# Performance work log

Measured on AMD Instinct MI355X. Metric: run time of the kernel, lower is better.

## Reference

```python
import jax, jax.numpy as jnp
import numpy as np
from jax import lax

B = 8192      # image batch
S = 32        # seq_length
I = 16        # ltc_input_size (sensory neurons)
U = 19        # ltc_hidden_size (units)
M = 2         # num_classes (motor neurons)
UNFOLDS = 6   # ncps LTCCell default ode_unfolds
EPS = 1e-8


def setup_inputs() -> dict:
    key = jax.random.key(0)
    ks = jax.random.split(key, 24)
    u = lambda k, sh, lo, hi: jax.random.uniform(k, sh, jnp.float32, lo, hi)
    x = jax.random.normal(ks[0], (B, 1, 28, 44), jnp.float32)
    conv1_w = jax.random.normal(ks[1], (6, 1, 5, 5), jnp.float32) * 0.2
    conv1_b = u(ks[2], (6,), -0.1, 0.1)
    conv2_w = jax.random.normal(ks[3], (16, 6, 5, 5), jnp.float32) * 0.08
    conv2_b = u(ks[4], (16,), -0.1, 0.1)
    # wiring adjacency (AutoNCP approximated by random sparse +/-1 polarity)
    sparsity_mask = (jax.random.uniform(ks[5], (U, U)) < 0.5).astype(jnp.float32)
    sensory_sparsity_mask = (jax.random.uniform(ks[6], (I, U)) < 0.5).astype(jnp.float32)
    erev = sparsity_mask * jnp.where(jax.random.uniform(ks[7], (U, U)) < 0.8, 1.0, -1.0)
    sensory_erev = sensory_sparsity_mask * jnp.where(jax.random.uniform(ks[8], (I, U)) < 0.8, 1.0, -1.0)
    # LTCCell parameter init ranges from ncps
    gleak = u(ks[9], (U,), 0.001, 1.0)
    vleak = u(ks[10], (U,), -0.2, 0.2)
    cm = u(ks[11], (U,), 0.4, 0.6)
    sigma = u(ks[12], (U, U), 3.0, 8.0)
    mu = u(ks[13], (U, U), 0.3, 0.8)
    w = u(ks[14], (U, U), 0.001, 1.0)
    sensory_sigma = u(ks[15], (I, U), 3.0, 8.0)
    sensory_mu = u(ks[16], (I, U), 0.3, 0.8)
    sensory_w = u(ks[17], (I, U), 0.001, 1.0)
    input_w = jnp.ones((I,), jnp.float32)
    input_b = jnp.zeros((I,), jnp.float32)
    output_w = jnp.ones((M,), jnp.float32)
    output_b = jnp.zeros((M,), jnp.float32)
    return dict(x=x, conv1_w=conv1_w, conv1_b=conv1_b, conv2_w=conv2_w, conv2_b=conv2_b,
                gleak=gleak, vleak=vleak, cm=cm, sigma=sigma, mu=mu, w=w, erev=erev,
                sensory_sigma=sensory_sigma, sensory_mu=sensory_mu, sensory_w=sensory_w,
                sensory_erev=sensory_erev, input_w=input_w, input_b=input_b,
                output_w=output_w, output_b=output_b,
                sparsity_mask=sparsity_mask, sensory_sparsity_mask=sensory_sparsity_mask)


def _maxpool2(h):
    return lax.reduce_window(h, -jnp.inf, lax.max, (1, 1, 2, 2), (1, 1, 2, 2), 'VALID')


def reference(x, conv1_w, conv1_b, conv2_w, conv2_b, gleak, vleak, cm, sigma, mu, w,
              erev, sensory_sigma, sensory_mu, sensory_w, sensory_erev, input_w, input_b,
              output_w, output_b, sparsity_mask, sensory_sparsity_mask):
    dn = ('NCHW', 'OIHW', 'NCHW')
    h = lax.conv_general_dilated(x, conv1_w, (1, 1), 'VALID', dimension_numbers=dn)
    h = _maxpool2(jax.nn.relu(h + conv1_b[None, :, None, None]))
    h = lax.conv_general_dilated(h, conv2_w, (1, 1), 'VALID', dimension_numbers=dn)
    h = _maxpool2(jax.nn.relu(h + conv2_b[None, :, None, None]))
    feat = h.reshape(h.shape[0], -1).reshape(-1, S, I)   # (B, 32, 16)
    seq = jnp.swapaxes(feat, 0, 1)                       # (S, B, I)
    cm_t = cm * UNFOLDS                                  # cm / (elapsed_time/unfolds), dt=1

    def step(v, inp):
        inp = inp * input_w + input_b                    # sensory affine mapping
        # sensory synapse activations (B, I, U), fixed over the ODE unfolds
        s_act = sensory_w * jax.nn.sigmoid(sensory_sigma * (inp[:, :, None] - sensory_mu))
        s_act = s_act * sensory_sparsity_mask
        w_num_s = jnp.sum(s_act * sensory_erev, axis=1)
        w_den_s = jnp.sum(s_act, axis=1)

        def unfold(vv, _):
            wa = w * jax.nn.sigmoid(sigma * (vv[:, :, None] - mu)) * sparsity_mask  # (B,U,U)
            num = cm_t * vv + gleak * vleak + jnp.sum(wa * erev, axis=1) + w_num_s
            den = cm_t + gleak + jnp.sum(wa, axis=1) + w_den_s
            return num / (den + EPS), None

        v, _ = lax.scan(unfold, v, None, length=UNFOLDS)
        return v, None

    v0 = jnp.zeros((feat.shape[0], U), x.dtype)
    vT, _ = lax.scan(step, v0, seq)
    # motor mapping: first M neurons, affine output map; equals out[:, -1, :]
    return vT[:, :M] * output_w + output_b
```

## Files before the change

### kernel.cpp

```cpp
#include <hip/hip_runtime.h>

#define BTOT 8192
#define SEQ 32
#define IPB 6
#define TPB 128
#define L2E 1.4426950408889634f
#define FSTRIDE 520
#define RSL 16


__global__ void prep_w2t(const float* __restrict__ w2, float* __restrict__ wt) {
    int idx = blockIdx.x * blockDim.x + threadIdx.x;
    if (idx < 2400) {
        int k = idx >> 4, c2 = idx & 15;
        wt[idx] = w2[c2 * 150 + k];
    }
}

__global__ void prep_params(
    const float* __restrict__ sigma, const float* __restrict__ mu,
    const float* __restrict__ ww, const float* __restrict__ erev,
    const float* __restrict__ ssigma, const float* __restrict__ smu,
    const float* __restrict__ sw, const float* __restrict__ serev,
    const float* __restrict__ inw, const float* __restrict__ inb,
    const float* __restrict__ mask, const float* __restrict__ smask,
    float* __restrict__ ws)
{
    __shared__ int mcol[19];
    float2* sAB = (float2*)(ws + 5632);
    float2* sZI = (float2*)(ws + 6240);
    int* cnt = (int*)(ws + 6848);
    float* Ap = ws + 7168;
    float* Bp = ws + 7680;
    float* Zp = ws + 8192;
    const int t = threadIdx.x;
    for (int idx = t; idx < 456; idx += 64) {
        int i = idx / 19, j = idx - (idx / 19) * 19;
        float a = 0.f, b = 0.f, z = 0.f;
        if (i < 19 && mask[i * 19 + j] != 0.f) {
            float s = sigma[i * 19 + j];
            a = -L2E * s;
            b = L2E * s * mu[i * 19 + j];
            z = ww[i * 19 + j] * erev[i * 19 + j];
        }
        Ap[idx] = a; Bp[idx] = b; Zp[idx] = z;
    }
    if (t < 19) {
        const int j = t;
        for (int c = 0; c < 16; ++c) {
            sAB[c * 19 + j] = make_float2(0.f, 0.f);
            sZI[c * 19 + j] = make_float2(0.f, __int_as_float(0));
        }
        int c = 0;
        for (int i = 0; i < 16; ++i) {
            int idx = i * 19 + j;
            if (smask[idx] != 0.f) {
                float s = ssigma[idx];
                sAB[c * 19 + j] = make_float2(-L2E * s * inw[i],
                                              -L2E * s * (inb[i] - smu[idx]));
                sZI[c * 19 + j] = make_float2(sw[idx] * serev[idx], __int_as_float(i));
                ++c;
            }
        }
        mcol[j] = c;
    }
    __syncthreads();
    if (t == 0) {
        int MS = 0;
        for (int k = 0; k < 19; ++k) MS = max(MS, mcol[k]);
        cnt[0] = 0;
        cnt[1] = MS;
    }
}

__global__ __launch_bounds__(128, 4) void conv_k(
    const float* __restrict__ xin,
    const float* __restrict__ w1, const float* __restrict__ b1,
    const float* __restrict__ b2, const float* __restrict__ wt,
    const float* __restrict__ sparam,
    const int* __restrict__ cnt,
    float2* __restrict__ wnwd)
{
    __shared__ __align__(16) float img[1232];
    __shared__ __align__(16) float c1p[1440];
    const int tid = threadIdx.x;
    const int bG = blockIdx.x;

    for (int idx = tid; idx < 1232; idx += 128) img[idx] = xin[bG * 1232 + idx];
    __syncthreads();
    for (int idx = tid; idx < 240; idx += 128) {
        int y = idx / 20, xx = idx - (idx / 20) * 20;
        const float* ib = img + (2 * y) * 44 + 2 * xx;
        float win[6][6];
        #pragma unroll
        for (int r = 0; r < 6; ++r) {
            float2 a = *(const float2*)(ib + r * 44);
            float2 b = *(const float2*)(ib + r * 44 + 2);
            float2 c = *(const float2*)(ib + r * 44 + 4);
            win[r][0] = a.x; win[r][1] = a.y; win[r][2] = b.x;
            win[r][3] = b.y; win[r][4] = c.x; win[r][5] = c.y;
        }
        for (int ch = 0; ch < 6; ++ch) {
            const float* wp = w1 + ch * 25;
            float a00 = 0.f, a01 = 0.f, a10 = 0.f, a11 = 0.f;
            #pragma unroll
            for (int ky = 0; ky < 5; ++ky)
                #pragma unroll
                for (int kx = 0; kx < 5; ++kx) {
                    float wv = wp[ky * 5 + kx];
                    a00 = fmaf(wv, win[ky][kx], a00);
                    a01 = fmaf(wv, win[ky][kx + 1], a01);
                    a10 = fmaf(wv, win[ky + 1][kx], a10);
                    a11 = fmaf(wv, win[ky + 1][kx + 1], a11);
                }
            float m = fmaxf(fmaxf(a00, a01), fmaxf(a10, a11)) + b1[ch];
            c1p[ch * 240 + idx] = fmaxf(m, 0.f);
        }
    }
    __syncthreads();
    {
        const int oy = tid >> 4, ox = tid & 15;
        float acc[16];
        #pragma unroll
        for (int c2 = 0; c2 < 16; ++c2) acc[c2] = 0.f;
        for (int ch = 0; ch < 6; ++ch) {
            const float* rowb = c1p + ch * 240 + oy * 20 + ox;
            const float* wch = wt + (ch * 25 << 4);
            #pragma unroll
            for (int ky = 0; ky < 5; ++ky) {
                #pragma unroll
                for (int kx = 0; kx < 5; ++kx) {
                    float xv = rowb[ky * 20 + kx];
                    const float4* wk = (const float4*)(wch + ((ky * 5 + kx) << 4));
                    float4 wa = wk[0], wb = wk[1], wc = wk[2], wd = wk[3];
                    acc[0]  = fmaf(wa.x, xv, acc[0]);  acc[1]  = fmaf(wa.y, xv, acc[1]);
                    acc[2]  = fmaf(wa.z, xv, acc[2]);  acc[3]  = fmaf(wa.w, xv, acc[3]);
                    acc[4]  = fmaf(wb.x, xv, acc[4]);  acc[5]  = fmaf(wb.y, xv, acc[5]);
                    acc[6]  = fmaf(wb.z, xv, acc[6]);  acc[7]  = fmaf(wb.w, xv, acc[7]);
                    acc[8]  = fmaf(wc.x, xv, acc[8]);  acc[9]  = fmaf(wc.y, xv, acc[9]);
                    acc[10] = fmaf(wc.z, xv, acc[10]); acc[11] = fmaf(wc.w, xv, acc[11]);
                    acc[12] = fmaf(wd.x, xv, acc[12]); acc[13] = fmaf(wd.y, xv, acc[13]);
                    acc[14] = fmaf(wd.z, xv, acc[14]); acc[15] = fmaf(wd.w, xv, acc[15]);
                }
            }
        }
        const bool wl = ((tid & 1) == 0) && ((tid & 16) == 0);
        const int obase = (oy >> 1) * 8 + (ox >> 1);
        #pragma unroll
        for (int c2 = 0; c2 < 16; ++c2) {
            float a = acc[c2];
            a = fmaxf(a, __shfl_xor(a, 1));
            a = fmaxf(a, __shfl_xor(a, 16));
            if (wl) img[obase + c2 * 32] = fmaxf(a + b2[c2], 0.f);
        }
    }
    __syncthreads();
    for (int idx = tid; idx < 1216; idx += 128) c1p[idx] = sparam[idx];
    __syncthreads();
    {
        const float2* sAB2 = (const float2*)c1p;
        const float2* sZI2 = (const float2*)(c1p + 608);
        const float* featI = img;
        const int MS = cnt[1];
        for (int p = tid; p < 608; p += 128) {
            int st = p / 19, j = p - (p / 19) * 19;
            float wn = 0.f, wd = 0.f;
            for (int c = 0; c < MS; ++c) {
                float2 ab = sAB2[c * 19 + j];
                float2 zi = sZI2[c * 19 + j];
                float f = featI[st * 16 + __float_as_int(zi.y)];
                float t = fmaf(ab.x, f, ab.y);
                float r = __builtin_amdgcn_rcpf(1.f + __builtin_amdgcn_exp2f(t));
                wn = fmaf(zi.x, r, wn);
                wd = fmaf(fabsf(zi.x), r, wd);
            }
            wnwd[(bG * SEQ + st) * 19 + j] = make_float2(wn, wd);
        }
    }
}

__global__ __launch_bounds__(128, 6) void ltc_k2(
    const float2* __restrict__ wnwd,
    const float* __restrict__ Ap, const float* __restrict__ Bp,
    const float* __restrict__ Zp,
    const float* __restrict__ gleak, const float* __restrict__ vleak,
    const float* __restrict__ cm,
    const float* __restrict__ outw, const float* __restrict__ outb,
    float* __restrict__ dout)
{
    __shared__ __align__(16) float vbuf[2][24];
    const int tid = threadIdx.x;
    const int wv = tid >> 6, l = tid & 63;
    const int s3 = l / 19;
    const int s = (s3 < 2) ? s3 : 2;
    const int j = l - s3 * 19;
    const int base = s * 8;
    const int img = blockIdx.x * 2 + wv;

    float A[8], Bb[8], Z[8];
    #pragma unroll
    for (int c = 0; c < 8; ++c) {
        A[c]  = Ap[(base + c) * 19 + j];
        Bb[c] = Bp[(base + c) * 19 + j];
        Z[c]  = Zp[(base + c) * 19 + j];
    }
    #pragma unroll
    for (int c = 0; c < 8; ++c)
        asm volatile("" : "+v"(A[c]), "+v"(Bb[c]), "+v"(Z[c]));

    const float gl = gleak[j];
    const float gv = gl * vleak[j];
    const float cmt = cm[j] * 6.f;

    float v = 0.f;
    float* vrow = &vbuf[wv][0];
    if (l < 24) vrow[l] = 0.f;
    __builtin_amdgcn_wave_barrier();
    __asm__ volatile("" ::: "memory");

    const float2* wrow = wnwd + img * SEQ * 19 + j;
    float2 wcur = wrow[0];

    #pragma unroll 1
    for (int st = 0; st < SEQ; ++st) {
        float2 wnext = (st < SEQ - 1) ? wrow[(st + 1) * 19] : wcur;
        const float nb = gv + wcur.x;
        const float db = cmt + gl + wcur.y;
        #pragma unroll 1
        for (int u = 0; u < 6; ++u) {
            float4 va = *(const float4*)(vrow + base);
            float4 vbq = *(const float4*)(vrow + base + 4);
            float vv[8] = {va.x, va.y, va.z, va.w, vbq.x, vbq.y, vbq.z, vbq.w};
            float pn0 = 0.f, pd0 = 0.f, pn1 = 0.f, pd1 = 0.f;
            #pragma unroll
            for (int p = 0; p < 4; ++p) {
                int c = p * 2;
                float t0 = fmaf(A[c], vv[c], Bb[c]);
                float t1 = fmaf(A[c + 1], vv[c + 1], Bb[c + 1]);
                float q0 = 1.f + __builtin_amdgcn_exp2f(t0);
                float q1 = 1.f + __builtin_amdgcn_exp2f(t1);
                float rr = __builtin_amdgcn_rcpf(q0 * q1);
                float cn = fmaf(Z[c], q1, Z[c + 1] * q0);
                float cd = fmaf(fabsf(Z[c]), q1, fabsf(Z[c + 1]) * q0);
                if (p & 1) { pn1 = fmaf(cn, rr, pn1); pd1 = fmaf(cd, rr, pd1); }
                else       { pn0 = fmaf(cn, rr, pn0); pd0 = fmaf(cd, rr, pd0); }
            }
            float pn = pn0 + pn1, pd = pd0 + pd1;
            float pnA = __shfl(pn, l + 19), pnB = __shfl(pn, l + 38);
            float pdA = __shfl(pd, l + 19), pdB = __shfl(pd, l + 38);
            float num = fmaf(cmt, v, nb) + (pn + pnA + pnB);
            float den = db + (pd + pdA + pdB);
            v = num * __builtin_amdgcn_rcpf(den + 1e-8f);
            __builtin_amdgcn_wave_barrier();
            __asm__ volatile("" ::: "memory");
            if (l < 19) vrow[l] = v;
            __builtin_amdgcn_wave_barrier();
            __asm__ volatile("" ::: "memory");
        }
        wcur = wnext;
    }
    if (l < 2) dout[img * 2 + l] = fmaf(v, outw[l], outb[l]);
}

__global__ __launch_bounds__(TPB, 3) void ltc_fused(
    const float* __restrict__ xin,
    const float* __restrict__ w1, const float* __restrict__ b1,
    const float* __restrict__ b2,
    const float* __restrict__ gleak, const float* __restrict__ vleak, const float* __restrict__ cm,
    const float* __restrict__ sigma, const float* __restrict__ mu, const float* __restrict__ ww,
    const float* __restrict__ erev,
    const float* __restrict__ ssigma, const float* __restrict__ smu, const float* __restrict__ sw,
    const float* __restrict__ serev,
    const float* __restrict__ inw, const float* __restrict__ inb,
    const float* __restrict__ outw, const float* __restrict__ outb,
    const float* __restrict__ mask, const float* __restrict__ smask,
    const float* __restrict__ wt,
    float* __restrict__ dout)
{
    __shared__ __align__(16) float uni[2736];
    __shared__ __align__(16) float featL[IPB * FSTRIDE];
    __shared__ int ncol[19], mcol[19], cnts[2];

    float* img = uni;
    float* c1p = uni + 1232;
    float2* rAB = (float2*)uni;
    float2* rZI = (float2*)(uni + 760);
    float2* sAB = (float2*)(uni + 1520);
    float2* sZI = (float2*)(uni + 2128);

    const int tid = threadIdx.x;
    const int b0 = blockIdx.x * IPB;

    for (int k = 0; k < IPB; ++k) {
        const int bG = b0 + k;
        const bool valid = bG < BTOT;
        if (valid) {
            for (int idx = tid; idx < 1232; idx += TPB) img[idx] = xin[bG * 1232 + idx];
        }
        __syncthreads();
        if (valid) {
            for (int idx = tid; idx < 240; idx += TPB) {
                int y = idx / 20, xx = idx - (idx / 20) * 20;
                const float* ib = img + (2 * y) * 44 + 2 * xx;
                float win[6][6];
                #pragma unroll
                for (int r = 0; r < 6; ++r) {
                    float2 a = *(const float2*)(ib + r * 44);
                    float2 b = *(const float2*)(ib + r * 44 + 2);
                    float2 c = *(const float2*)(ib + r * 44 + 4);
                    win[r][0] = a.x; win[r][1] = a.y; win[r][2] = b.x;
                    win[r][3] = b.y; win[r][4] = c.x; win[r][5] = c.y;
                }
                for (int ch = 0; ch < 6; ++ch) {
                    const float* wp = w1 + ch * 25;
                    float a00 = 0.f, a01 = 0.f, a10 = 0.f, a11 = 0.f;
                    #pragma unroll
                    for (int ky = 0; ky < 5; ++ky)
                        #pragma unroll
                        for (int kx = 0; kx < 5; ++kx) {
                            float wv = wp[ky * 5 + kx];
                            a00 = fmaf(wv, win[ky][kx], a00);
                            a01 = fmaf(wv, win[ky][kx + 1], a01);
                            a10 = fmaf(wv, win[ky + 1][kx], a10);
                            a11 = fmaf(wv, win[ky + 1][kx + 1], a11);
                        }
                    float m = fmaxf(fmaxf(a00, a01), fmaxf(a10, a11)) + b1[ch];
                    c1p[ch * 240 + idx] = fmaxf(m, 0.f);
                }
            }
        }
        __syncthreads();
        if (valid) {
            const int oy = tid >> 4, ox = tid & 15;
            float acc[16];
            #pragma unroll
            for (int c2 = 0; c2 < 16; ++c2) acc[c2] = 0.f;
            for (int ch = 0; ch < 6; ++ch) {
                const float* rowb = c1p + ch * 240 + oy * 20 + ox;
                const float* wch = wt + (ch * 25 << 4);
                #pragma unroll
                for (int ky = 0; ky < 5; ++ky) {
                    #pragma unroll
                    for (int kx = 0; kx < 5; ++kx) {
                        float xv = rowb[ky * 20 + kx];
                        const float4* wk = (const float4*)(wch + ((ky * 5 + kx) << 4));
                        float4 wa = wk[0], wb = wk[1], wc = wk[2], wd = wk[3];
                        acc[0]  = fmaf(wa.x, xv, acc[0]);  acc[1]  = fmaf(wa.y, xv, acc[1]);
                        acc[2]  = fmaf(wa.z, xv, acc[2]);  acc[3]  = fmaf(wa.w, xv, acc[3]);
                        acc[4]  = fmaf(wb.x, xv, acc[4]);  acc[5]  = fmaf(wb.y, xv, acc[5]);
                        acc[6]  = fmaf(wb.z, xv, acc[6]);  acc[7]  = fmaf(wb.w, xv, acc[7]);
                        acc[8]  = fmaf(wc.x, xv, acc[8]);  acc[9]  = fmaf(wc.y, xv, acc[9]);
                        acc[10] = fmaf(wc.z, xv, acc[10]); acc[11] = fmaf(wc.w, xv, acc[11]);
                        acc[12] = fmaf(wd.x, xv, acc[12]); acc[13] = fmaf(wd.y, xv, acc[13]);
                        acc[14] = fmaf(wd.z, xv, acc[14]); acc[15] = fmaf(wd.w, xv, acc[15]);
                    }
                }
            }
            const bool wl = ((tid & 1) == 0) && ((tid & 16) == 0);
            const int obase = k * FSTRIDE + (oy >> 1) * 8 + (ox >> 1);
            #pragma unroll
            for (int c2 = 0; c2 < 16; ++c2) {
                float a = acc[c2];
                a = fmaxf(a, __shfl_xor(a, 1));
                a = fmaxf(a, __shfl_xor(a, 16));
                if (wl) featL[obase + c2 * 32] = fmaxf(a + b2[c2], 0.f);
            }
        }
        __syncthreads();
    }

    for (int idx = tid; idx < 2736; idx += TPB) uni[idx] = 0.f;
    __syncthreads();
    if (tid < 19) {
        const int jj = tid;
        int c = 0;
        for (int i = 0; i < 19; ++i) {
            int idx = i * 19 + jj;
            if (mask[idx] != 0.f) {
                float s = sigma[idx];
                rAB[c * 19 + jj] = make_float2(-L2E * s, L2E * s * mu[idx]);
                rZI[c * 19 + jj] = make_float2(ww[idx] * erev[idx], __int_as_float(i));
                ++c;
            }
        }
        ncol[jj] = c;
        c = 0;
        for (int i = 0; i < 16; ++i) {
            int idx = i * 19 + jj;
            if (smask[idx] != 0.f) {
                float s = ssigma[idx];
                sAB[c * 19 + jj] = make_float2(-L2E * s * inw[i],
                                               -L2E * s * (inb[i] - smu[idx]));
                sZI[c * 19 + jj] = make_float2(sw[idx] * serev[idx], __int_as_float(i));
                ++c;
            }
        }
        mcol[jj] = c;
    }
    __syncthreads();
    if (tid == 0) {
        int MRv = 0, MSv = 0;
        for (int j2 = 0; j2 < 19; ++j2) {
            MRv = max(MRv, ncol[j2]);
            MSv = max(MSv, mcol[j2]);
        }
        cnts[0] = MRv;
        cnts[1] = MSv;
    }
    __syncthreads();
    const int MR = __builtin_amdgcn_readfirstlane(cnts[0]);
    const int MS = __builtin_amdgcn_readfirstlane(cnts[1]);

    const int wv_ = tid >> 6, l = tid & 63;
    const int g = l / 19;
    const int j = l - g * 19;
    const int gbase = g * 19;
    const int kimg = wv_ * 3 + g;
    const bool act = (g < 3) && (b0 + kimg < BTOT);
    const int kc = (kimg < IPB) ? kimg : (IPB - 1);

    float UA[RSL], UB[RSL], UZ[RSL];
    int LI[RSL];
    #pragma unroll
    for (int c = 0; c < RSL; ++c) {
        float2 ab = rAB[c * 19 + j];
        float2 zi = rZI[c * 19 + j];
        UA[c] = ab.x; UB[c] = ab.y; UZ[c] = zi.x;
        LI[c] = gbase + __float_as_int(zi.y);
    }
    #pragma unroll
    for (int c = 0; c < RSL; ++c)
        asm volatile("" : "+v"(UA[c]), "+v"(UB[c]), "+v"(UZ[c]), "+v"(LI[c]));

    const float gl = gleak[j];
    const float gv = gl * vleak[j];
    const float cmt = cm[j] * 6.f;

    float v = 0.f;
    const float* frow = featL + kc * FSTRIDE;

    #pragma unroll 1
    for (int st = 0; st < SEQ; ++st) {
        const float* fb = frow + st * 16;
        float wns = 0.f, wds = 0.f;
        #pragma unroll 1
        for (int c = 0; c < MS; ++c) {
            float2 ab = sAB[c * 19 + j];
            float2 zi = sZI[c * 19 + j];
            float f = fb[__float_as_int(zi.y)];
            float t = fmaf(ab.x, f, ab.y);
            float r = __builtin_amdgcn_rcpf(1.f + __builtin_amdgcn_exp2f(t));
            wns = fmaf(zi.x, r, wns);
            wds = fmaf(fabsf(zi.x), r, wds);
        }
        const float nb = gv + wns;
        const float db = cmt + gl + wds;
        #pragma unroll 1
        for (int u = 0; u < 6; ++u) {
            float num = fmaf(cmt, v, nb);
            float den = db;
            #pragma unroll
            for (int c = 0; c < RSL; ++c) {
                float vv = __shfl(v, LI[c]);
                float t = fmaf(UA[c], vv, UB[c]);
                float r = __builtin_amdgcn_rcpf(1.f + __builtin_amdgcn_exp2f(t));
                num = fmaf(UZ[c], r, num);
                den = fmaf(fabsf(UZ[c]), r, den);
            }
            #pragma unroll 1
            for (int c = RSL; c < MR; ++c) {
                float2 ab = rAB[c * 19 + j];
                float2 zi = rZI[c * 19 + j];
                float vv = __shfl(v, gbase + __float_as_int(zi.y));
                float t = fmaf(ab.x, vv, ab.y);
                float r = __builtin_amdgcn_rcpf(1.f + __builtin_amdgcn_exp2f(t));
                num = fmaf(zi.x, r, num);
                den = fmaf(fabsf(zi.x), r, den);
            }
            v = num * __builtin_amdgcn_rcpf(den + 1e-8f);
        }
    }
    if (act && j < 2) dout[(b0 + kimg) * 2 + j] = fmaf(v, outw[j], outb[j]);
}

extern "C" void kernel_launch(void* const* d_in, const int* in_sizes, int n_in,
                              void* d_out, int out_size, void* d_ws, size_t ws_size,
                              hipStream_t stream) {
    const float* x      = (const float*)d_in[0];
    const float* w1     = (const float*)d_in[1];
    const float* b1     = (const float*)d_in[2];
    const float* w2     = (const float*)d_in[3];
    const float* b2     = (const float*)d_in[4];
    const float* gleak  = (const float*)d_in[5];
    const float* vleak  = (const float*)d_in[6];
    const float* cm     = (const float*)d_in[7];
    const float* sigma  = (const float*)d_in[8];
    const float* mu     = (const float*)d_in[9];
    const float* ww     = (const float*)d_in[10];
    const float* erev   = (const float*)d_in[11];
    const float* ssig   = (const float*)d_in[12];
    const float* smu    = (const float*)d_in[13];
    const float* sw     = (const float*)d_in[14];
    const float* serev  = (const float*)d_in[15];
    const float* inw    = (const float*)d_in[16];
    const float* inb    = (const float*)d_in[17];
    const float* outw   = (const float*)d_in[18];
    const float* outb   = (const float*)d_in[19];
    const float* mask   = (const float*)d_in[20];
    const float* smask  = (const float*)d_in[21];

    float* ws = (float*)d_ws;
    const size_t need = (size_t)(12288 + (size_t)BTOT * SEQ * 19 * 2) * 4;

    hipLaunchKernelGGL(prep_w2t, dim3(10), dim3(256), 0, stream, w2, ws);

    if (ws_size >= need) {
        hipLaunchKernelGGL(prep_params, dim3(1), dim3(64), 0, stream,
                           sigma, mu, ww, erev, ssig, smu, sw, serev, inw, inb,
                           mask, smask, ws);
        hipLaunchKernelGGL(conv_k, dim3(BTOT), dim3(128), 0, stream,
                           x, w1, b1, b2, (const float*)ws,
                           (const float*)(ws + 5632), (const int*)(ws + 6848),
                           (float2*)(ws + 12288));
        hipLaunchKernelGGL(ltc_k2, dim3(BTOT / 2), dim3(128), 0, stream,
                           (const float2*)(ws + 12288),
                           (const float*)(ws + 7168), (const float*)(ws + 7680),
                           (const float*)(ws + 8192),
                           gleak, vleak, cm, outw, outb, (float*)d_out);
    } else {
        hipLaunchKernelGGL(ltc_fused, dim3((BTOT + IPB - 1) / IPB), dim3(TPB), 0, stream,
                           x, w1, b1, b2, gleak, vleak, cm, sigma, mu, ww, erev,
                           ssig, smu, sw, serev, inw, inb, outw, outb, mask, smask,
                           (const float*)ws, (float*)d_out);
    }
}
```

Baseline: 346.1 us.

## Fuse conv/sensory kernel with LTC recurrence kernel, keep wnwd in LDS

Merges the conv+sensory-activation kernel and the LTC recurrence kernel into a single kernel in which each block handles two images. The per-timestep sensory sums now stay in shared memory instead of making a round trip through a large global workspace, and one kernel launch is removed. In exchange, the sparam table is read from global/cache instead of being staged in LDS. The recurrence phase also uses only two waves per block, so the conv and recurrence phases can no longer overlap across kernels, and occupancy now has to serve both phases.

```diff
diff --git a/kernel.cpp b/kernel.cpp
--- a/kernel.cpp
+++ b/kernel.cpp
@@ -73,97 +73,110 @@
     }
 }
 
-__global__ __launch_bounds__(128, 4) void conv_k(
+__global__ __launch_bounds__(128, 5) void fused2(
     const float* __restrict__ xin,
     const float* __restrict__ w1, const float* __restrict__ b1,
     const float* __restrict__ b2, const float* __restrict__ wt,
     const float* __restrict__ sparam,
     const int* __restrict__ cnt,
-    float2* __restrict__ wnwd)
+    const float* __restrict__ Ap, const float* __restrict__ Bp,
+    const float* __restrict__ Zp,
+    const float* __restrict__ gleak, const float* __restrict__ vleak,
+    const float* __restrict__ cm,
+    const float* __restrict__ outw, const float* __restrict__ outb,
+    float* __restrict__ dout)
 {
-    __shared__ __align__(16) float img[1232];
-    __shared__ __align__(16) float c1p[1440];
+    __shared__ __align__(16) float uni[2672];
+    __shared__ __align__(16) float featL[2][512];
+    __shared__ __align__(16) float vbuf[2][24];
+
+    float* img = uni;
+    float* c1p = uni + 1232;
     const int tid = threadIdx.x;
-    const int bG = blockIdx.x;
-
-    for (int idx = tid; idx < 1232; idx += 128) img[idx] = xin[bG * 1232 + idx];
-    __syncthreads();
-    for (int idx = tid; idx < 240; idx += 128) {
-        int y = idx / 20, xx = idx - (idx / 20) * 20;
-        const float* ib = img + (2 * y) * 44 + 2 * xx;
-        float win[6][6];
-        #pragma unroll
-        for (int r = 0; r < 6; ++r) {
-            float2 a = *(const float2*)(ib + r * 44);
-            float2 b = *(const float2*)(ib + r * 44 + 2);
-            float2 c = *(const float2*)(ib + r * 44 + 4);
-            win[r][0] = a.x; win[r][1] = a.y; win[r][2] = b.x;
-            win[r][3] = b.y; win[r][4] = c.x; win[r][5] = c.y;
-        }
-        for (int ch = 0; ch < 6; ++ch) {
-            const float* wp = w1 + ch * 25;
-            float a00 = 0.f, a01 = 0.f, a10 = 0.f, a11 = 0.f;
-            #pragma unroll
-            for (int ky = 0; ky < 5; ++ky)
+    const int b0 = blockIdx.x * 2;
+
+    for (int k = 0; k < 2; ++k) {
+        const int bG = b0 + k;
+        for (int idx = tid; idx < 1232; idx += 128) img[idx] = xin[bG * 1232 + idx];
+        __syncthreads();
+        for (int idx = tid; idx < 240; idx += 128) {
+            int y = idx / 20, xx = idx - (idx / 20) * 20;
+            const float* ib = img + (2 * y) * 44 + 2 * xx;
+            float win[6][6];
+            #pragma unroll
+            for (int r = 0; r < 6; ++r) {
+                float2 a = *(const float2*)(ib + r * 44);
+                float2 b = *(const float2*)(ib + r * 44 + 2);
+                float2 c = *(const float2*)(ib + r * 44 + 4);
+                win[r][0] = a.x; win[r][1] = a.y; win[r][2] = b.x;
+                win[r][3] = b.y; win[r][4] = c.x; win[r][5] = c.y;
+            }
+            for (int ch = 0; ch < 6; ++ch) {
+                const float* wp = w1 + ch * 25;
+                float a00 = 0.f, a01 = 0.f, a10 = 0.f, a11 = 0.f;
                 #pragma unroll
-                for (int kx = 0; kx < 5; ++kx) {
-                    float wv = wp[ky * 5 + kx];
-                    a00 = fmaf(wv, win[ky][kx], a00);
-                    a01 = fmaf(wv, win[ky][kx + 1], a01);
-                    a10 = fmaf(wv, win[ky + 1][kx], a10);
-                    a11 = fmaf(wv, win[ky + 1][kx + 1], a11);
+                for (int ky = 0; ky < 5; ++ky)
+                    #pragma unroll
+                    for (int kx = 0; kx < 5; ++kx) {
+                        float wv = wp[ky * 5 + kx];
+                        a00 = fmaf(wv, win[ky][kx], a00);
+                        a01 = fmaf(wv, win[ky][kx + 1], a01);
+                        a10 = fmaf(wv, win[ky + 1][kx], a10);
+                        a11 = fmaf(wv, win[ky + 1][kx + 1], a11);
+                    }
+                float m = fmaxf(fmaxf(a00, a01), fmaxf(a10, a11)) + b1[ch];
+                c1p[ch * 240 + idx] = fmaxf(m, 0.f);
+            }
+        }
+        __syncthreads();
+        {
+            const int oy = tid >> 4, ox = tid & 15;
+            float acc[16];
+            #pragma unroll
+            for (int c2 = 0; c2 < 16; ++c2) acc[c2] = 0.f;
+            for (int ch = 0; ch < 6; ++ch) {
+                const float* rowb = c1p + ch * 240 + oy * 20 + ox;
+                const float* wch = wt + (ch * 25 << 4);
+                #pragma unroll
+                for (int ky = 0; ky < 5; ++ky) {
+                    #pragma unroll
+                    for (int kx = 0; kx < 5; ++kx) {
+                        float xv = rowb[ky * 20 + kx];
+                        const float4* wk = (const float4*)(wch + ((ky * 5 + kx) << 4));
+                        float4 wa = wk[0], wb = wk[1], wc = wk[2], wd = wk[3];
+                        acc[0]  = fmaf(wa.x, xv, acc[0]);  acc[1]  = fmaf(wa.y, xv, acc[1]);
+                        acc[2]  = fmaf(wa.z, xv, acc[2]);  acc[3]  = fmaf(wa.w, xv, acc[3]);
+                        acc[4]  = fmaf(wb.x, xv, acc[4]);  acc[5]  = fmaf(wb.y, xv, acc[5]);
+                        acc[6]  = fmaf(wb.z, xv, acc[6]);  acc[7]  = fmaf(wb.w, xv, acc[7]);
+                        acc[8]  = fmaf(wc.x, xv, acc[8]);  acc[9]  = fmaf(wc.y, xv, acc[9]);
+                        acc[10] = fmaf(wc.z, xv, acc[10]); acc[11] = fmaf(wc.w, xv, acc[11]);
+                        acc[12] = fmaf(wd.x, xv, acc[12]); acc[13] = fmaf(wd.y, xv, acc[13]);
+                        acc[14] = fmaf(wd.z, xv, acc[14]); acc[15] = fmaf(wd.w, xv, acc[15]);
+                    }
                 }
-            float m = fmaxf(fmaxf(a00, a01), fmaxf(a10, a11)) + b1[ch];
-            c1p[ch * 240 + idx] = fmaxf(m, 0.f);
-        }
-    }
-    __syncthreads();
+            }
+            const bool wl = ((tid & 1) == 0) && ((tid & 16) == 0);
+            const int obase = (oy >> 1) * 8 + (ox >> 1);
+            #pragma unroll
+            for (int c2 = 0; c2 < 16; ++c2) {
+                float a = acc[c2];
+                a = fmaxf(a, __shfl_xor(a, 1));
+                a = fmaxf(a, __shfl_xor(a, 16));
+                if (wl) featL[k][obase + c2 * 32] = fmaxf(a + b2[c2], 0.f);
+            }
+        }
+        __syncthreads();
+    }
+
+    float2* wnwdL = (float2*)uni;
     {
-        const int oy = tid >> 4, ox = tid & 15;
-        float acc[16];
-        #pragma unroll
-        for (int c2 = 0; c2 < 16; ++c2) acc[c2] = 0.f;
-        for (int ch = 0; ch < 6; ++ch) {
-            const float* rowb = c1p + ch * 240 + oy * 20 + ox;
-            const float* wch = wt + (ch * 25 << 4);
-            #pragma unroll
-            for (int ky = 0; ky < 5; ++ky) {
-                #pragma unroll
-                for (int kx = 0; kx < 5; ++kx) {
-                    float xv = rowb[ky * 20 + kx];
-                    const float4* wk = (const float4*)(wch + ((ky * 5 + kx) << 4));
-                    float4 wa = wk[0], wb = wk[1], wc = wk[2], wd = wk[3];
-                    acc[0]  = fmaf(wa.x, xv, acc[0]);  acc[1]  = fmaf(wa.y, xv, acc[1]);
-                    acc[2]  = fmaf(wa.z, xv, acc[2]);  acc[3]  = fmaf(wa.w, xv, acc[3]);
-                    acc[4]  = fmaf(wb.x, xv, acc[4]);  acc[5]  = fmaf(wb.y, xv, acc[5]);
-                    acc[6]  = fmaf(wb.z, xv, acc[6]);  acc[7]  = fmaf(wb.w, xv, acc[7]);
-                    acc[8]  = fmaf(wc.x, xv, acc[8]);  acc[9]  = fmaf(wc.y, xv, acc[9]);
-                    acc[10] = fmaf(wc.z, xv, acc[10]); acc[11] = fmaf(wc.w, xv, acc[11]);
-                    acc[12] = fmaf(wd.x, xv, acc[12]); acc[13] = fmaf(wd.y, xv, acc[13]);
-                    acc[14] = fmaf(wd.z, xv, acc[14]); acc[15] = fmaf(wd.w, xv, acc[15]);
-                }
-            }
-        }
-        const bool wl = ((tid & 1) == 0) && ((tid & 16) == 0);
-        const int obase = (oy >> 1) * 8 + (ox >> 1);
-        #pragma unroll
-        for (int c2 = 0; c2 < 16; ++c2) {
-            float a = acc[c2];
-            a = fmaxf(a, __shfl_xor(a, 1));
-            a = fmaxf(a, __shfl_xor(a, 16));
-            if (wl) img[obase + c2 * 32] = fmaxf(a + b2[c2], 0.f);
-        }
-    }
-    __syncthreads();
-    for (int idx = tid; idx < 1216; idx += 128) c1p[idx] = sparam[idx];
-    __syncthreads();
-    {
-        const float2* sAB2 = (const float2*)c1p;
-        const float2* sZI2 = (const float2*)(c1p + 608);
-        const float* featI = img;
+        const float2* sAB2 = (const float2*)sparam;
+        const float2* sZI2 = (const float2*)(sparam + 608);
         const int MS = cnt[1];
-        for (int p = tid; p < 608; p += 128) {
-            int st = p / 19, j = p - (p / 19) * 19;
+        for (int p = tid; p < 1216; p += 128) {
+            int k = p / 608, q = p - (p / 608) * 608;
+            int st = q / 19, j = q - (q / 19) * 19;
+            const float* featI = featL[k];
             float wn = 0.f, wd = 0.f;
             for (int c = 0; c < MS; ++c) {
                 float2 ab = sAB2[c * 19 + j];
@@ -174,28 +187,17 @@
                 wn = fmaf(zi.x, r, wn);
                 wd = fmaf(fabsf(zi.x), r, wd);
             }
-            wnwd[(bG * SEQ + st) * 19 + j] = make_float2(wn, wd);
-        }
-    }
-}
-
-__global__ __launch_bounds__(128, 6) void ltc_k2(
-    const float2* __restrict__ wnwd,
-    const float* __restrict__ Ap, const float* __restrict__ Bp,
-    const float* __restrict__ Zp,
-    const float* __restrict__ gleak, const float* __restrict__ vleak,
-    const float* __restrict__ cm,
-    const float* __restrict__ outw, const float* __restrict__ outb,
-    float* __restrict__ dout)
-{
-    __shared__ __align__(16) float vbuf[2][24];
-    const int tid = threadIdx.x;
+            wnwdL[p] = make_float2(wn, wd);
+        }
+    }
+    __syncthreads();
+
     const int wv = tid >> 6, l = tid & 63;
     const int s3 = l / 19;
     const int s = (s3 < 2) ? s3 : 2;
     const int j = l - s3 * 19;
     const int base = s * 8;
-    const int img = blockIdx.x * 2 + wv;
+    const int imgi = b0 + wv;
 
     float A[8], Bb[8], Z[8];
     #pragma unroll
@@ -218,12 +220,11 @@
     __builtin_amdgcn_wave_barrier();
     __asm__ volatile("" ::: "memory");
 
-    const float2* wrow = wnwd + img * SEQ * 19 + j;
-    float2 wcur = wrow[0];
+    const float2* wrow = wnwdL + wv * 608 + j;
 
     #pragma unroll 1
     for (int st = 0; st < SEQ; ++st) {
-        float2 wnext = (st < SEQ - 1) ? wrow[(st + 1) * 19] : wcur;
+        float2 wcur = wrow[st * 19];
         const float nb = gv + wcur.x;
         const float db = cmt + gl + wcur.y;
         #pragma unroll 1
@@ -257,9 +258,8 @@
             __builtin_amdgcn_wave_barrier();
             __asm__ volatile("" ::: "memory");
         }
-        wcur = wnext;
-    }
-    if (l < 2) dout[img * 2 + l] = fmaf(v, outw[l], outb[l]);
+    }
+    if (l < 2) dout[imgi * 2 + l] = fmaf(v, outw[l], outb[l]);
 }
 
 __global__ __launch_bounds__(TPB, 3) void ltc_fused(
@@ -510,7 +510,7 @@
     const float* smask  = (const float*)d_in[21];
 
     float* ws = (float*)d_ws;
-    const size_t need = (size_t)(12288 + (size_t)BTOT * SEQ * 19 * 2) * 4;
+    const size_t need = (size_t)12288 * 4;
 
     hipLaunchKernelGGL(prep_w2t, dim3(10), dim3(256), 0, stream, w2, ws);
 
@@ -518,12 +518,9 @@
         hipLaunchKernelGGL(prep_params, dim3(1), dim3(64), 0, stream,
                            sigma, mu, ww, erev, ssig, smu, sw, serev, inw, inb,
                            mask, smask, ws);
-        hipLaunchKernelGGL(conv_k, dim3(BTOT), dim3(128), 0, stream,
+        hipLaunchKernelGGL(fused2, dim3(BTOT / 2), dim3(128), 0, stream,
                            x, w1, b1, b2, (const float*)ws,
                            (const float*)(ws + 5632), (const int*)(ws + 6848),
-                           (float2*)(ws + 12288));
-        hipLaunchKernelGGL(ltc_k2, dim3(BTOT / 2), dim3(128), 0, stream,
-                           (const float2*)(ws + 12288),
                            (const float*)(ws + 7168), (const float*)(ws + 7680),
                            (const float*)(ws + 8192),
                            gleak, vleak, cm, outw, outb, (float*)d_out);
```

Result: no change. 349.4 us (+0.9%).
